# Optimization experiments

Hardware: AMD Instinct MI355X
Metric: run time of the kernel (lower is better)

## Reference

```python
import jax, jax.numpy as jnp
import numpy as np

IN_DIM, OUT_DIM, NUM_KNOTS = 256, 256, 20
X_MIN, X_MAX = -5.0, 5.0
H = (X_MAX - X_MIN) / (NUM_KNOTS - 1)  # uniform knot spacing


def setup_inputs() -> dict:
    key = jax.random.key(0)
    k1, k2 = jax.random.split(key, 2)
    x = jax.random.normal(k1, (1024, IN_DIM), dtype=jnp.float32) * 2.0
    # per-(out,in)-pair cubic coefficients for each of the NUM_KNOTS-1 intervals: [a,b,c,d]
    coeffs = jax.random.normal(k2, (OUT_DIM, IN_DIM, NUM_KNOTS - 1, 4), dtype=jnp.float32) * 0.1
    bias = jnp.zeros((OUT_DIM,), dtype=jnp.float32)
    return {"x": x, "coeffs": coeffs, "bias": bias}


def reference(x, coeffs, bias):
    # x: [B, I]; coeffs: [J, I, K, 4]; bias: [J]
    B, I = x.shape
    K = coeffs.shape[2]
    # locate knot interval (clamped -> linear-cubic extrapolation at edges)
    idx = jnp.clip(jnp.floor((x - X_MIN) / H).astype(jnp.int32), 0, K - 1)  # [B, I]
    t = x - (X_MIN + idx.astype(x.dtype) * H)                               # [B, I]
    # gather per-pair interval coefficients: [J, B, I, 4]
    i_arr = jnp.broadcast_to(jnp.arange(I)[None, :], idx.shape)
    c = coeffs[:, i_arr, idx]
    a, b, c2, d = c[..., 0], c[..., 1], c[..., 2], c[..., 3]
    # Horner evaluation; t broadcasts [B,I] -> [J,B,I]
    y = ((d * t + c2) * t + b) * t + a
    # sum over input dims, add bias: [B, J]
    return y.sum(axis=-1).T + bias[None, :]
```

## Files before the change

### kernel.cpp

```cpp
#include <hip/hip_runtime.h>

#define IN_DIM   256
#define OUT_DIM  256
#define NKNOT    19
#define X_MIN_C  (-5.0f)
#define H_C      (10.0f / 19.0f)
#define INV_H_C  (19.0f / 10.0f)

__global__ __launch_bounds__(256) void transpose_coeffs(
        const float4* __restrict__ src, float4* __restrict__ dst) {
    __shared__ float4 tile[64][65];
    const int c0 = (blockIdx.x % 76) * 64;
    const int r0 = (blockIdx.x / 76) * 64;
    const int tx = threadIdx.x & 63;
    const int ty = threadIdx.x >> 6;

    #pragma unroll
    for (int jj = 0; jj < 16; ++jj) {
        const int r = ty * 16 + jj;
        tile[tx][r] = src[(size_t)(r0 + r) * 4864 + (size_t)(c0 + tx)];
    }
    __syncthreads();
    #pragma unroll
    for (int jj = 0; jj < 16; ++jj) {
        const int c = ty * 16 + jj;
        dst[(size_t)(c0 + c) * 256 + (size_t)(r0 + tx)] = tile[c][tx];
    }
}

__global__ __launch_bounds__(256) void kan_main(
        const float*  __restrict__ x,
        const float4* __restrict__ Ct,
        const float*  __restrict__ bias,
        float*        __restrict__ out) {
    __shared__ int   s_koff[IN_DIM];
    __shared__ float s_t[IN_DIM];

    const int b = blockIdx.x;
    const int o = threadIdx.x;

    {
        const float xv = x[b * IN_DIM + o];
        const float f  = (xv - X_MIN_C) * INV_H_C;
        int idx = (int)floorf(f);
        idx = idx < 0 ? 0 : (idx > NKNOT - 1 ? NKNOT - 1 : idx);
        s_koff[o] = idx * 256;
        s_t[o]    = xv - (X_MIN_C + (float)idx * H_C);
    }
    __syncthreads();

    const float4* base = Ct + o;
    float acc0 = 0.f, acc1 = 0.f, acc2 = 0.f, acc3 = 0.f;

    #pragma unroll 4
    for (int i = 0; i < IN_DIM; i += 4) {
        const float t0 = s_t[i + 0];
        const float t1 = s_t[i + 1];
        const float t2 = s_t[i + 2];
        const float t3 = s_t[i + 3];
        const float4 c0 = base[(i + 0) * (NKNOT * 256) + s_koff[i + 0]];
        const float4 c1 = base[(i + 1) * (NKNOT * 256) + s_koff[i + 1]];
        const float4 c2 = base[(i + 2) * (NKNOT * 256) + s_koff[i + 2]];
        const float4 c3 = base[(i + 3) * (NKNOT * 256) + s_koff[i + 3]];
        acc0 += ((c0.w * t0 + c0.z) * t0 + c0.y) * t0 + c0.x;
        acc1 += ((c1.w * t1 + c1.z) * t1 + c1.y) * t1 + c1.x;
        acc2 += ((c2.w * t2 + c2.z) * t2 + c2.y) * t2 + c2.x;
        acc3 += ((c3.w * t3 + c3.z) * t3 + c3.y) * t3 + c3.x;
    }

    out[b * OUT_DIM + o] = bias[o] + ((acc0 + acc1) + (acc2 + acc3));
}

extern "C" void kernel_launch(void* const* d_in, const int* in_sizes, int n_in,
                              void* d_out, int out_size, void* d_ws, size_t ws_size,
                              hipStream_t stream) {
    const float* x      = (const float*)d_in[0];
    const float* coeffs = (const float*)d_in[1];
    const float* bias   = (const float*)d_in[2];
    float*       out    = (float*)d_out;

    const int B = in_sizes[0] / IN_DIM;
    float4* Ct = (float4*)d_ws;

    transpose_coeffs<<<304, 256, 0, stream>>>((const float4*)coeffs, Ct);
    kan_main<<<B, 256, 0, stream>>>(x, Ct, bias, out);
}
```

Measured before the change: 115.6 us.

## Stage bf16-packed coefficient slices in LDS with split-K partial sums

Replaces the transpose+gather kernel with a pack kernel that converts coefficients to bf16 and tiles them into per-(output-group, input-group) slices, a precompute kernel for interval index and offset t, a main kernel that loads each slice into LDS and evaluates cubic splines for 64-batch chunks, and a reduction kernel summing partials across input groups plus bias. The aim is to replace scattered global float4 gathers with LDS lookups and to halve coefficient bytes. It adds extra launches, a partial-sum buffer, and bf16 rounding error in the coefficients.

After: 144.3 us. +24.9%, slower.

```diff
diff --git a/kernel.cpp b/kernel.cpp
--- a/kernel.cpp
+++ b/kernel.cpp
@@ -7,68 +7,141 @@
 #define H_C      (10.0f / 19.0f)
 #define INV_H_C  (19.0f / 10.0f)
 
-__global__ __launch_bounds__(256) void transpose_coeffs(
-        const float4* __restrict__ src, float4* __restrict__ dst) {
-    __shared__ float4 tile[64][65];
-    const int c0 = (blockIdx.x % 76) * 64;
-    const int r0 = (blockIdx.x / 76) * 64;
-    const int tx = threadIdx.x & 63;
-    const int ty = threadIdx.x >> 6;
+#define ROWS     5
+#define PLANE_E  (8 * NKNOT * ROWS)
+#define SLICE_E  (2 * PLANE_E)
 
-    #pragma unroll
-    for (int jj = 0; jj < 16; ++jj) {
-        const int r = ty * 16 + jj;
-        tile[tx][r] = src[(size_t)(r0 + r) * 4864 + (size_t)(c0 + tx)];
+__device__ __forceinline__ unsigned int pk_bf16(float x, float y) {
+    unsigned int ux = __float_as_uint(x); ux += 0x7FFFu + ((ux >> 16) & 1u);
+    unsigned int uy = __float_as_uint(y); uy += 0x7FFFu + ((uy >> 16) & 1u);
+    return (ux >> 16) | (uy & 0xFFFF0000u);
+}
+__device__ __forceinline__ float lo16(unsigned int u) { return __uint_as_float(u << 16); }
+__device__ __forceinline__ float hi16(unsigned int u) { return __uint_as_float(u & 0xFFFF0000u); }
+
+__global__ __launch_bounds__(256) void pack_coeffs(
+        const float4* __restrict__ src, uint4* __restrict__ dst) {
+    __shared__ float4 buf[16 * NKNOT];
+    const int g = blockIdx.x & 15;
+    const int i = blockIdx.x >> 4;
+
+    for (int e = threadIdx.x; e < 16 * NKNOT; e += 256) {
+        const int o_l = e / NKNOT, k = e - o_l * NKNOT;
+        buf[e] = src[((size_t)(g * 16 + o_l) * IN_DIM + i) * NKNOT + k];
     }
     __syncthreads();
-    #pragma unroll
-    for (int jj = 0; jj < 16; ++jj) {
-        const int c = ty * 16 + jj;
-        dst[(size_t)(c0 + c) * 256 + (size_t)(r0 + tx)] = tile[c][tx];
+
+    const int t = threadIdx.x;
+    if (t < 2 * 76) {
+        const int plane = t / 76;
+        const int r     = t - plane * 76;
+        const int k = r >> 2, og = r & 3;
+        const float4 v0 = buf[(og * 4 + 0) * NKNOT + k];
+        const float4 v1 = buf[(og * 4 + 1) * NKNOT + k];
+        const float4 v2 = buf[(og * 4 + 2) * NKNOT + k];
+        const float4 v3 = buf[(og * 4 + 3) * NKNOT + k];
+        uint4 w;
+        if (plane == 0) {
+            w.x = pk_bf16(v0.x, v1.x); w.y = pk_bf16(v2.x, v3.x);
+            w.z = pk_bf16(v0.y, v1.y); w.w = pk_bf16(v2.y, v3.y);
+        } else {
+            w.x = pk_bf16(v0.z, v1.z); w.y = pk_bf16(v2.z, v3.z);
+            w.z = pk_bf16(v0.w, v1.w); w.w = pk_bf16(v2.w, v3.w);
+        }
+        const int i_grp = i >> 3, i_l = i & 7;
+        dst[(size_t)(g * 32 + i_grp) * SLICE_E + plane * PLANE_E
+            + (i_l * NKNOT + k) * ROWS + og] = w;
     }
 }
 
-__global__ __launch_bounds__(256) void kan_main(
-        const float*  __restrict__ x,
-        const float4* __restrict__ Ct,
-        const float*  __restrict__ bias,
-        float*        __restrict__ out) {
-    __shared__ int   s_koff[IN_DIM];
-    __shared__ float s_t[IN_DIM];
+__global__ __launch_bounds__(256) void make_tk(
+        const float* __restrict__ x, int2* __restrict__ tkg, int Btot) {
+    const int n = blockIdx.x * 256 + threadIdx.x;
+    if (n >= Btot * IN_DIM) return;
+    const int b = n >> 8, i = n & 255;
+    const float xv = x[n];
+    int idx = (int)floorf((xv - X_MIN_C) * INV_H_C);
+    idx = idx < 0 ? 0 : (idx > NKNOT - 1 ? NKNOT - 1 : idx);
+    tkg[((size_t)(i >> 3) * Btot + b) * 8 + (i & 7)] =
+        make_int2(idx * ROWS, __float_as_int(xv - (X_MIN_C + (float)idx * H_C)));
+}
 
-    const int b = blockIdx.x;
-    const int o = threadIdx.x;
+__global__ __launch_bounds__(256, 4) void kan_main(
+        const int2*  __restrict__ tkg,
+        const uint4* __restrict__ Ct,
+        float4*      __restrict__ part,
+        int Btot) {
+    __shared__ uint4 cs[SLICE_E];
+    __shared__ int2  stk[64 * 9];
 
-    {
-        const float xv = x[b * IN_DIM + o];
-        const float f  = (xv - X_MIN_C) * INV_H_C;
-        int idx = (int)floorf(f);
-        idx = idx < 0 ? 0 : (idx > NKNOT - 1 ? NKNOT - 1 : idx);
-        s_koff[o] = idx * 256;
-        s_t[o]    = xv - (X_MIN_C + (float)idx * H_C);
+    const int g     = blockIdx.x & 15;
+    const int i_grp = (blockIdx.x >> 4) & 31;
+    const int bh    = blockIdx.x >> 9;
+    const int tid   = threadIdx.x;
+
+    const uint4* slice = Ct + (size_t)(g * 32 + i_grp) * SLICE_E;
+    for (int e = tid; e < SLICE_E; e += 256) cs[e] = slice[e];
+
+    const int b_l = tid >> 2;
+    const int og  = tid & 3;
+    const uint4* ab = cs + og;
+    const uint4* cd = cs + PLANE_E + og;
+
+    const int half    = Btot >> 1;
+    const int nchunks = half >> 6;
+
+    for (int c = 0; c < nchunks; ++c) {
+        const int bbase = bh * half + c * 64;
+        __syncthreads();
+        {
+            const size_t tb = ((size_t)i_grp * Btot + bbase) * 8;
+            int e = tid;
+            stk[(e >> 3) * 9 + (e & 7)] = tkg[tb + e];
+            e += 256;
+            stk[(e >> 3) * 9 + (e & 7)] = tkg[tb + e];
+        }
+        __syncthreads();
+
+        float y0 = 0.f, y1 = 0.f, y2 = 0.f, y3 = 0.f;
+        #pragma unroll
+        for (int i = 0; i < 8; ++i) {
+            const int2 tk = stk[b_l * 9 + i];
+            const int  e  = i * (NKNOT * ROWS) + tk.x;
+            const uint4 AB = ab[e];
+            const uint4 CD = cd[e];
+            const float t  = __int_as_float(tk.y);
+            const float a_0 = lo16(AB.x), a_1 = hi16(AB.x), a_2 = lo16(AB.y), a_3 = hi16(AB.y);
+            const float b_0 = lo16(AB.z), b_1 = hi16(AB.z), b_2 = lo16(AB.w), b_3 = hi16(AB.w);
+            const float c_0 = lo16(CD.x), c_1 = hi16(CD.x), c_2 = lo16(CD.y), c_3 = hi16(CD.y);
+            const float d_0 = lo16(CD.z), d_1 = hi16(CD.z), d_2 = lo16(CD.w), d_3 = hi16(CD.w);
+            y0 += ((d_0 * t + c_0) * t + b_0) * t + a_0;
+            y1 += ((d_1 * t + c_1) * t + b_1) * t + a_1;
+            y2 += ((d_2 * t + c_2) * t + b_2) * t + a_2;
+            y3 += ((d_3 * t + c_3) * t + b_3) * t + a_3;
+        }
+
+        part[((size_t)(i_grp * 16 + g) * Btot + bbase + b_l) * 4 + og] =
+            make_float4(y0, y1, y2, y3);
     }
-    __syncthreads();
+}
 
-    const float4* base = Ct + o;
-    float acc0 = 0.f, acc1 = 0.f, acc2 = 0.f, acc3 = 0.f;
-
-    #pragma unroll 4
-    for (int i = 0; i < IN_DIM; i += 4) {
-        const float t0 = s_t[i + 0];
-        const float t1 = s_t[i + 1];
-        const float t2 = s_t[i + 2];
-        const float t3 = s_t[i + 3];
-        const float4 c0 = base[(i + 0) * (NKNOT * 256) + s_koff[i + 0]];
-        const float4 c1 = base[(i + 1) * (NKNOT * 256) + s_koff[i + 1]];
-        const float4 c2 = base[(i + 2) * (NKNOT * 256) + s_koff[i + 2]];
-        const float4 c3 = base[(i + 3) * (NKNOT * 256) + s_koff[i + 3]];
-        acc0 += ((c0.w * t0 + c0.z) * t0 + c0.y) * t0 + c0.x;
-        acc1 += ((c1.w * t1 + c1.z) * t1 + c1.y) * t1 + c1.x;
-        acc2 += ((c2.w * t2 + c2.z) * t2 + c2.y) * t2 + c2.x;
-        acc3 += ((c3.w * t3 + c3.z) * t3 + c3.y) * t3 + c3.x;
+__global__ __launch_bounds__(256) void kan_reduce(
+        const float4* __restrict__ part,
+        const float4* __restrict__ bias4,
+        float4*       __restrict__ out,
+        int Btot) {
+    const int n = blockIdx.x * 256 + threadIdx.x;
+    if (n >= Btot * 64) return;
+    const int b  = n >> 6;
+    const int g  = (n >> 2) & 15;
+    const int og = n & 3;
+    float4 s = bias4[n & 63];
+    #pragma unroll 8
+    for (int i_grp = 0; i_grp < 32; ++i_grp) {
+        const float4 p = part[((size_t)(i_grp * 16 + g) * Btot + b) * 4 + og];
+        s.x += p.x; s.y += p.y; s.z += p.z; s.w += p.w;
     }
-
-    out[b * OUT_DIM + o] = bias[o] + ((acc0 + acc1) + (acc2 + acc3));
+    out[n] = s;
 }
 
 extern "C" void kernel_launch(void* const* d_in, const int* in_sizes, int n_in,
@@ -79,9 +152,14 @@
     const float* bias   = (const float*)d_in[2];
     float*       out    = (float*)d_out;
 
-    const int B = in_sizes[0] / IN_DIM;
-    float4* Ct = (float4*)d_ws;
+    const int Btot = in_sizes[0] / IN_DIM;
+    uint4* Ct   = (uint4*)d_ws;
+    int2*  tkg  = (int2*)((char*)d_ws + (16u << 20));
+    float* part = (float*)((char*)d_ws + (32u << 20));
 
-    transpose_coeffs<<<304, 256, 0, stream>>>((const float4*)coeffs, Ct);
-    kan_main<<<B, 256, 0, stream>>>(x, Ct, bias, out);
+    pack_coeffs<<<16 * IN_DIM, 256, 0, stream>>>((const float4*)coeffs, Ct);
+    make_tk<<<(Btot * IN_DIM + 255) / 256, 256, 0, stream>>>(x, tkg, Btot);
+    kan_main<<<1024, 256, 0, stream>>>(tkg, Ct, (float4*)part, Btot);
+    kan_reduce<<<(Btot * 64 + 255) / 256, 256, 0, stream>>>(
+        (const float4*)part, (const float4*)bias, (float4*)out, Btot);
 }
```
